# Kernel tuning notes

Hardware: AMD Instinct MI355X
Metric: run time of the kernel (lower is better)

Reference implementation:

```python
import jax, jax.numpy as jnp
import numpy as np

NUM_HEADS = 16
D_MODEL = 1024


def setup_inputs() -> dict:
    key = jax.random.key(0)
    k1, k2, k3 = jax.random.split(key, 3)
    x = jax.random.normal(k1, (4, 2048, D_MODEL), dtype=jnp.float32)
    # torch.nn.Linear weights are [out_features, in_features]
    w_qkv = jax.random.normal(k2, (3 * D_MODEL, D_MODEL), dtype=jnp.float32) * (1.0 / np.sqrt(D_MODEL))
    w_o = jax.random.normal(k3, (D_MODEL, D_MODEL), dtype=jnp.float32) * (1.0 / np.sqrt(D_MODEL))
    return {"x": x, "w_qkv": w_qkv, "w_o": w_o}


def reference(x, w_qkv, w_o):
    b, n, _ = x.shape
    h = NUM_HEADS
    dh = D_MODEL // h  # head dim
    qkv = jnp.einsum('bnd,ed->bne', x, w_qkv)            # (b, n, 3*d_model)
    # Faithful to: rearrange(qkv, 'b n (h d) -> b h n d', h=h) then chunk(3, dim=-1)
    qkv = qkv.reshape(b, n, h, 3 * dh).transpose(0, 2, 1, 3)  # (b, h, n, 3*dh)
    q, k, v = jnp.split(qkv, 3, axis=-1)                 # each (b, h, n, dh)
    scale = 1.0 / jnp.sqrt(jnp.asarray(dh, dtype=x.dtype))
    scores = jnp.einsum('bhqd,bhkd->bhqk', q, k) * scale  # (b, h, n, n)
    attn = jax.nn.softmax(scores, axis=-1)
    out = jnp.einsum('bhqk,bhkd->bhqd', attn, v)          # (b, h, n, dh)
    out = out.transpose(0, 2, 1, 3).reshape(b, n, h * dh)  # 'b h n d -> b n (h d)'
    return jnp.einsum('bnd,ed->bne', out, w_o)
```

## Files before the change

kernel.cpp:

```cpp
#include <hip/hip_runtime.h>

#define BATCH 4
#define SEQ 2048
#define DM 1024
#define NH 16
#define DH 64
#define M_TOT (BATCH * SEQ)
#define EQKV (3 * DM)
#define QSCALE 0.18033688011112042f

typedef __bf16 bf16x8 __attribute__((ext_vector_type(8)));
typedef unsigned short u16x8 __attribute__((ext_vector_type(8)));
typedef float f32x4 __attribute__((ext_vector_type(4)));
typedef float f32x16 __attribute__((ext_vector_type(16)));

static __device__ __forceinline__ unsigned short f2bf(float f) {
    unsigned int u = __builtin_bit_cast(unsigned int, f);
    u += 0x7fffu + ((u >> 16) & 1u);
    return (unsigned short)(u >> 16);
}

static __device__ __forceinline__ unsigned short f2bf_fast(float f) {
    return (unsigned short)((__builtin_bit_cast(unsigned int, f) + 0x8000u) >> 16);
}

static __device__ __forceinline__ unsigned int pkbf_fast(float a, float b) {
    unsigned int ua = __builtin_bit_cast(unsigned int, a) + 0x8000u;
    unsigned int ub = __builtin_bit_cast(unsigned int, b) + 0x8000u;
#if __has_builtin(__builtin_amdgcn_perm)
    return __builtin_amdgcn_perm(ub, ua, 0x07060302u);
#else
    return (ua >> 16) | (ub & 0xFFFF0000u);
#endif
}

static __device__ __forceinline__ float fast_exp2(float x) {
#if __has_builtin(__builtin_amdgcn_exp2f)
    return __builtin_amdgcn_exp2f(x);
#else
    return exp2f(x);
#endif
}

static __device__ __forceinline__ bf16x8 ld_frag(const ushort* p) {
    return *(const bf16x8*)p;
}

static __device__ __forceinline__ bf16x8 mk_frag(unsigned int a, unsigned int b,
                                                 unsigned int c, unsigned int d) {
    union { unsigned int u[4]; bf16x8 v; } t;
    t.u[0] = a; t.u[1] = b; t.u[2] = c; t.u[3] = d;
    return t.v;
}

__global__ __launch_bounds__(256) void detect_kernel(const ushort* __restrict__ x,
                                                     int* __restrict__ flag) {
    __shared__ int cnt[256];
    const int tid = threadIdx.x;
    int c = 0;
    for (int j = 0; j < 16; ++j) {
        unsigned short w = x[tid * 16 + j];
        int e = (w >> 7) & 0xFF;
        bool sane = (e == 0) || (e >= 0x60 && e <= 0x8F);
        c += sane ? 0 : 1;
    }
    cnt[tid] = c;
    __syncthreads();
    for (int s = 128; s > 0; s >>= 1) {
        if (tid < s) cnt[tid] += cnt[tid + s];
        __syncthreads();
    }
    if (tid == 0) flag[0] = (cnt[0] > 256) ? 1 : 0;
}

__global__ __launch_bounds__(256) void convert_frag_kernel(
    const void* __restrict__ src, ushort* __restrict__ dst, int R,
    const int* __restrict__ flag)
{
    const int t = blockIdx.x * 256 + threadIdx.x;
    if (t >= R * 128) return;
    const int m = t >> 7, kc = t & 127;

    u16x8 v;
    if (flag[0]) {
        const float* s = (const float*)src + (size_t)t * 8;
        #pragma unroll
        for (int j = 0; j < 8; ++j) v[j] = f2bf(s[j]);
    } else {
        v = *((const u16x8*)src + t);
    }
    const size_t o = (((size_t)(m >> 4) * 32 + (kc >> 2)) * 64 + (kc & 3) * 16 + (m & 15)) * 8;
    *(u16x8*)(dst + o) = v;
}

__global__ __launch_bounds__(256) void qkv_gemm_kernel(
    const ushort* __restrict__ XF, const ushort* __restrict__ WF,
    ushort* __restrict__ QF, ushort* __restrict__ KF, ushort* __restrict__ VF)
{
    const int lane = threadIdx.x & 63;
    const int wave = threadIdx.x >> 6;
    const int col  = lane & 15;
    const int quad = lane >> 4;
    const int m0 = blockIdx.y * 128 + (wave >> 1) * 64;
    const int e0 = blockIdx.x * 128 + (wave & 1) * 64;
    const int mt0 = m0 >> 4, et0 = e0 >> 4;

    f32x4 acc[4][4];
    #pragma unroll
    for (int i = 0; i < 4; ++i)
        #pragma unroll
        for (int j = 0; j < 4; ++j) acc[i][j] = f32x4{0.f, 0.f, 0.f, 0.f};

    for (int kt = 0; kt < 32; ++kt) {
        bf16x8 a[4], b[4];
        #pragma unroll
        for (int i = 0; i < 4; ++i) {
            a[i] = ld_frag(XF + ((size_t)((mt0 + i) * 32 + kt) * 64 + lane) * 8);
            b[i] = ld_frag(WF + ((size_t)((et0 + i) * 32 + kt) * 64 + lane) * 8);
        }
        #pragma unroll
        for (int i = 0; i < 4; ++i)
            #pragma unroll
            for (int j = 0; j < 4; ++j)
                acc[i][j] = __builtin_amdgcn_mfma_f32_16x16x32_bf16(a[i], b[j], acc[i][j], 0, 0, 0);
    }

    #pragma unroll
    for (int ej = 0; ej < 4; ++ej) {
        const int e = e0 + ej * 16 + col;
        const int h = e / 192;
        const int c = e - h * 192;
        #pragma unroll
        for (int mi = 0; mi < 4; ++mi) {
            #pragma unroll
            for (int r = 0; r < 4; ++r) {
                const int m = m0 + mi * 16 + quad * 4 + r;
                const int bh = (m >> 11) * NH + h;
                const int n = m & (SEQ - 1);
                const float val = acc[mi][ej][r];
                if (c < 64) {
                    const int d = c;
                    QF[(((size_t)(bh * 64 + (n >> 5)) * 4 + (d >> 4)) * 64
                        + ((d >> 3) & 1) * 32 + (n & 31)) * 8 + (d & 7)] = f2bf_fast(val * QSCALE);
                } else if (c < 128) {
                    const int d = c - 64;
                    KF[(((size_t)(bh * 64 + (n >> 5)) * 4 + (d >> 4)) * 64
                        + ((d >> 3) & 1) * 32 + (n & 31)) * 8 + (d & 7)] = f2bf_fast(val);
                } else {
                    const int d = c - 128;
                    const int r4 = n & 15;
                    const int s4 = (r4 & 3) | (((r4 >> 3) & 1) << 2) | (((r4 >> 2) & 1) << 3);
                    VF[((((size_t)(bh * 32 + (n >> 6)) * 2 + (d >> 5)) * 4 + ((n >> 4) & 3)) * 64
                        + (s4 >> 3) * 32 + (d & 31)) * 8 + (s4 & 7)] = f2bf_fast(val);
                }
            }
        }
    }
}

__global__ __launch_bounds__(256) void attn_kernel(
    const ushort* __restrict__ QF, const ushort* __restrict__ KF,
    const ushort* __restrict__ VF, ushort* __restrict__ AOF)
{
    __shared__ float lred[2][33][64];

    const int lane = threadIdx.x & 63;
    const int wave = threadIdx.x >> 6;
    const int half = lane >> 5;
    const int l31  = lane & 31;

    const int i = blockIdx.x;
    const int xcd = i & 7;
    const int s = i >> 3;
    const int qc = s & 31;
    const int bh = ((s >> 5) << 3) | xcd;
    const int qt  = wave & 1;
    const int kvh = wave >> 1;
    const int q0 = qc * 64 + qt * 32;

    const ushort* qfb = QF + ((size_t)(bh * 64 + (q0 >> 5)) * 4) * 512;
    bf16x8 bq[4];
    #pragma unroll
    for (int d4 = 0; d4 < 4; ++d4) bq[d4] = ld_frag(qfb + d4 * 512 + lane * 8);

    const ushort* kfb = KF + (size_t)bh * 131072 + (size_t)kvh * 65536;
    const ushort* vfb = VF + (size_t)bh * 131072 + (size_t)kvh * 65536;

    float l_i = 0.f;
    f32x16 acc0 = {}, acc1 = {};

    for (int it = 0; it < 16; ++it) {
        const ushort* vp = vfb + (size_t)it * 4096;
        bf16x8 va0[4], va1[4];
        #pragma unroll
        for (int f4 = 0; f4 < 4; ++f4) {
            va0[f4] = ld_frag(vp + f4 * 512 + lane * 8);
            va1[f4] = ld_frag(vp + (4 + f4) * 512 + lane * 8);
        }

        f32x16 st0 = {}, st1 = {};
        const ushort* kp = kfb + (size_t)it * 4096;
        #pragma unroll
        for (int d4 = 0; d4 < 4; ++d4) {
            bf16x8 ka0 = ld_frag(kp + d4 * 512 + lane * 8);
            bf16x8 ka1 = ld_frag(kp + (4 + d4) * 512 + lane * 8);
            st0 = __builtin_amdgcn_mfma_f32_32x32x16_bf16(ka0, bq[d4], st0, 0, 0, 0);
            st1 = __builtin_amdgcn_mfma_f32_32x32x16_bf16(ka1, bq[d4], st1, 0, 0, 0);
        }

        float rs = 0.f;
        #pragma unroll
        for (int t = 0; t < 16; ++t) { st0[t] = fast_exp2(st0[t]); rs += st0[t]; }
        #pragma unroll
        for (int t = 0; t < 16; ++t) { st1[t] = fast_exp2(st1[t]); rs += st1[t]; }
        l_i += rs;

        bf16x8 pf[4];
        pf[0] = mk_frag(pkbf_fast(st0[0],  st0[1]),  pkbf_fast(st0[2],  st0[3]),
                        pkbf_fast(st0[4],  st0[5]),  pkbf_fast(st0[6],  st0[7]));
        pf[1] = mk_frag(pkbf_fast(st0[8],  st0[9]),  pkbf_fast(st0[10], st0[11]),
                        pkbf_fast(st0[12], st0[13]), pkbf_fast(st0[14], st0[15]));
        pf[2] = mk_frag(pkbf_fast(st1[0],  st1[1]),  pkbf_fast(st1[2],  st1[3]),
                        pkbf_fast(st1[4],  st1[5]),  pkbf_fast(st1[6],  st1[7]));
        pf[3] = mk_frag(pkbf_fast(st1[8],  st1[9]),  pkbf_fast(st1[10], st1[11]),
                        pkbf_fast(st1[12], st1[13]), pkbf_fast(st1[14], st1[15]));

        #pragma unroll
        for (int f4 = 0; f4 < 4; ++f4) {
            acc0 = __builtin_amdgcn_mfma_f32_32x32x16_bf16(va0[f4], pf[f4], acc0, 0, 0, 0);
            acc1 = __builtin_amdgcn_mfma_f32_32x32x16_bf16(va1[f4], pf[f4], acc1, 0, 0, 0);
        }
    }

    l_i += __shfl_xor(l_i, 32, 64);

    if (kvh == 1) {
        #pragma unroll
        for (int r = 0; r < 16; ++r) {
            lred[qt][r][lane]      = acc0[r];
            lred[qt][16 + r][lane] = acc1[r];
        }
        lred[qt][32][lane] = l_i;
    }
    __syncthreads();
    if (kvh == 0) {
        #pragma unroll
        for (int r = 0; r < 16; ++r) {
            acc0[r] += lred[qt][r][lane];
            acc1[r] += lred[qt][16 + r][lane];
        }
        l_i += lred[qt][32][lane];

        const int b = bh >> 4, h = bh & (NH - 1);
        const float inv = 1.f / l_i;
        const int n_g = b * SEQ + q0 + l31;
        #pragma unroll
        for (int r = 0; r < 16; ++r) {
            const int d = (r & 3) + 8 * (r >> 2) + 4 * half;
            #pragma unroll
            for (int p = 0; p < 2; ++p) {
                const int e = h * 64 + p * 32 + d;
                const float val = (p == 0 ? acc0[r] : acc1[r]) * inv;
                AOF[(((size_t)(n_g >> 4) * 32 + (e >> 5)) * 64
                     + ((e >> 3) & 3) * 16 + (n_g & 15)) * 8 + (e & 7)] = f2bf_fast(val);
            }
        }
    }
}

__global__ __launch_bounds__(256) void out_gemm_kernel(
    const ushort* __restrict__ AOF, const ushort* __restrict__ WOF,
    void* __restrict__ out, const int* __restrict__ flag)
{
    const int lane = threadIdx.x & 63;
    const int wave = threadIdx.x >> 6;
    const int col  = lane & 15;
    const int quad = lane >> 4;
    const int m0 = blockIdx.y * 128 + (wave >> 1) * 64;
    const int e0 = blockIdx.x * 128 + (wave & 1) * 64;
    const int mt0 = m0 >> 4, et0 = e0 >> 4;
    const int f = flag[0];

    f32x4 acc[4][4];
    #pragma unroll
    for (int i = 0; i < 4; ++i)
        #pragma unroll
        for (int j = 0; j < 4; ++j) acc[i][j] = f32x4{0.f, 0.f, 0.f, 0.f};

    for (int kt = 0; kt < 32; ++kt) {
        bf16x8 a[4], b[4];
        #pragma unroll
        for (int i = 0; i < 4; ++i) {
            a[i] = ld_frag(AOF + ((size_t)((mt0 + i) * 32 + kt) * 64 + lane) * 8);
            b[i] = ld_frag(WOF + ((size_t)((et0 + i) * 32 + kt) * 64 + lane) * 8);
        }
        #pragma unroll
        for (int i = 0; i < 4; ++i)
            #pragma unroll
            for (int j = 0; j < 4; ++j)
                acc[i][j] = __builtin_amdgcn_mfma_f32_16x16x32_bf16(a[i], b[j], acc[i][j], 0, 0, 0);
    }

    if (f == 0) {
        ushort* o = (ushort*)out;
        #pragma unroll
        for (int mi = 0; mi < 4; ++mi)
            #pragma unroll
            for (int ej = 0; ej < 4; ++ej)
                #pragma unroll
                for (int r = 0; r < 4; ++r)
                    o[(size_t)(m0 + mi * 16 + quad * 4 + r) * DM + e0 + ej * 16 + col] = f2bf_fast(acc[mi][ej][r]);
    } else {
        float* o = (float*)out;
        #pragma unroll
        for (int mi = 0; mi < 4; ++mi)
            #pragma unroll
            for (int ej = 0; ej < 4; ++ej)
                #pragma unroll
                for (int r = 0; r < 4; ++r)
                    o[(size_t)(m0 + mi * 16 + quad * 4 + r) * DM + e0 + ej * 16 + col] = acc[mi][ej][r];
    }
}

extern "C" void kernel_launch(void* const* d_in, const int* in_sizes, int n_in,
                              void* d_out, int out_size, void* d_ws, size_t ws_size,
                              hipStream_t stream) {
    const void* x_raw     = d_in[0];
    const void* w_qkv_raw = d_in[1];
    const void* w_o_raw   = d_in[2];

    char* ws = (char*)d_ws;
    int*    flag  = (int*)ws;
    ushort* XF    = (ushort*)(ws + 256);
    ushort* WQKVF = (ushort*)(ws + 256 + (16u << 20));
    ushort* WOF   = (ushort*)(ws + 256 + (22u << 20));
    ushort* QF    = (ushort*)(ws + 256 + (24u << 20));
    ushort* KF    = (ushort*)(ws + 256 + (40u << 20));
    ushort* VF    = (ushort*)(ws + 256 + (56u << 20));
    ushort* AOF   = XF;

    detect_kernel<<<1, 256, 0, stream>>>((const ushort*)x_raw, flag);
    convert_frag_kernel<<<M_TOT / 2, 256, 0, stream>>>(x_raw, XF, M_TOT, flag);
    convert_frag_kernel<<<EQKV / 2, 256, 0, stream>>>(w_qkv_raw, WQKVF, EQKV, flag);
    convert_frag_kernel<<<DM / 2, 256, 0, stream>>>(w_o_raw, WOF, DM, flag);

    qkv_gemm_kernel<<<dim3(EQKV / 128, M_TOT / 128), 256, 0, stream>>>(XF, WQKVF, QF, KF, VF);
    attn_kernel<<<dim3(BATCH * NH * (SEQ / 64)), 256, 0, stream>>>(QF, KF, VF, AOF);
    out_gemm_kernel<<<dim3(DM / 128, M_TOT / 128), 256, 0, stream>>>(AOF, WOF, d_out, flag);
}
```

Measured before the change: 302.8 us.

## Swizzle GEMM block order per XCD and use packed bf16 convert and adds

Both projection GEMMs remap block indices so that blocks landing on the same XCD work on a contiguous tile region, which aims to improve L2 reuse of the operand tiles. In the attention kernel, the bf16 packing of the exp2 probabilities now uses the hardware v_cvt_pk_bf16_f32 instruction instead of manual bit arithmetic. The row-sum accumulation uses packed v_pk_add_f32 across four partial accumulators, which cuts VALU instruction count and shortens the dependency chain. Rounding changes from round-half-up to the hardware's rounding mode, and the ordering of the sum changes slightly.

```diff
diff --git a/kernel.cpp b/kernel.cpp
--- a/kernel.cpp
+++ b/kernel.cpp
@@ -11,6 +11,7 @@
 
 typedef __bf16 bf16x8 __attribute__((ext_vector_type(8)));
 typedef unsigned short u16x8 __attribute__((ext_vector_type(8)));
+typedef float f32x2 __attribute__((ext_vector_type(2)));
 typedef float f32x4 __attribute__((ext_vector_type(4)));
 typedef float f32x16 __attribute__((ext_vector_type(16)));
 
@@ -24,14 +25,16 @@
     return (unsigned short)((__builtin_bit_cast(unsigned int, f) + 0x8000u) >> 16);
 }
 
-static __device__ __forceinline__ unsigned int pkbf_fast(float a, float b) {
-    unsigned int ua = __builtin_bit_cast(unsigned int, a) + 0x8000u;
-    unsigned int ub = __builtin_bit_cast(unsigned int, b) + 0x8000u;
-#if __has_builtin(__builtin_amdgcn_perm)
-    return __builtin_amdgcn_perm(ub, ua, 0x07060302u);
-#else
-    return (ua >> 16) | (ub & 0xFFFF0000u);
-#endif
+static __device__ __forceinline__ unsigned int cvt_pk_bf16(float lo, float hi) {
+    unsigned int r;
+    asm("v_cvt_pk_bf16_f32 %0, %1, %2" : "=v"(r) : "v"(lo), "v"(hi));
+    return r;
+}
+
+static __device__ __forceinline__ f32x2 pk_add(f32x2 a, f32x2 b) {
+    f32x2 d;
+    asm("v_pk_add_f32 %0, %1, %2" : "=v"(d) : "v"(a), "v"(b));
+    return d;
 }
 
 static __device__ __forceinline__ float fast_exp2(float x) {
@@ -101,8 +104,12 @@
     const int wave = threadIdx.x >> 6;
     const int col  = lane & 15;
     const int quad = lane >> 4;
-    const int m0 = blockIdx.y * 128 + (wave >> 1) * 64;
-    const int e0 = blockIdx.x * 128 + (wave & 1) * 64;
+    const int orig = blockIdx.y * 24 + blockIdx.x;
+    const int sid  = (orig & 7) * 192 + (orig >> 3);
+    const int bx = sid % 24;
+    const int by = sid / 24;
+    const int m0 = by * 128 + (wave >> 1) * 64;
+    const int e0 = bx * 128 + (wave & 1) * 64;
     const int mt0 = m0 >> 4, et0 = e0 >> 4;
 
     f32x4 acc[4][4];
@@ -186,8 +193,19 @@
     const ushort* kfb = KF + (size_t)bh * 131072 + (size_t)kvh * 65536;
     const ushort* vfb = VF + (size_t)bh * 131072 + (size_t)kvh * 65536;
 
-    float l_i = 0.f;
+    f32x2 lp0 = {0.f, 0.f}, lp1 = {0.f, 0.f}, lp2 = {0.f, 0.f}, lp3 = {0.f, 0.f};
     f32x16 acc0 = {}, acc1 = {};
+
+#define LACC(v) do { \
+        lp0 = pk_add(lp0, __builtin_shufflevector(v, v, 0, 1));   \
+        lp1 = pk_add(lp1, __builtin_shufflevector(v, v, 2, 3));   \
+        lp2 = pk_add(lp2, __builtin_shufflevector(v, v, 4, 5));   \
+        lp3 = pk_add(lp3, __builtin_shufflevector(v, v, 6, 7));   \
+        lp0 = pk_add(lp0, __builtin_shufflevector(v, v, 8, 9));   \
+        lp1 = pk_add(lp1, __builtin_shufflevector(v, v, 10, 11)); \
+        lp2 = pk_add(lp2, __builtin_shufflevector(v, v, 12, 13)); \
+        lp3 = pk_add(lp3, __builtin_shufflevector(v, v, 14, 15)); \
+    } while (0)
 
     for (int it = 0; it < 16; ++it) {
         const ushort* vp = vfb + (size_t)it * 4096;
@@ -208,22 +226,22 @@
             st1 = __builtin_amdgcn_mfma_f32_32x32x16_bf16(ka1, bq[d4], st1, 0, 0, 0);
         }
 
-        float rs = 0.f;
-        #pragma unroll
-        for (int t = 0; t < 16; ++t) { st0[t] = fast_exp2(st0[t]); rs += st0[t]; }
-        #pragma unroll
-        for (int t = 0; t < 16; ++t) { st1[t] = fast_exp2(st1[t]); rs += st1[t]; }
-        l_i += rs;
+        #pragma unroll
+        for (int t = 0; t < 16; ++t) st0[t] = fast_exp2(st0[t]);
+        #pragma unroll
+        for (int t = 0; t < 16; ++t) st1[t] = fast_exp2(st1[t]);
+        LACC(st0);
+        LACC(st1);
 
         bf16x8 pf[4];
-        pf[0] = mk_frag(pkbf_fast(st0[0],  st0[1]),  pkbf_fast(st0[2],  st0[3]),
-                        pkbf_fast(st0[4],  st0[5]),  pkbf_fast(st0[6],  st0[7]));
-        pf[1] = mk_frag(pkbf_fast(st0[8],  st0[9]),  pkbf_fast(st0[10], st0[11]),
-                        pkbf_fast(st0[12], st0[13]), pkbf_fast(st0[14], st0[15]));
-        pf[2] = mk_frag(pkbf_fast(st1[0],  st1[1]),  pkbf_fast(st1[2],  st1[3]),
-                        pkbf_fast(st1[4],  st1[5]),  pkbf_fast(st1[6],  st1[7]));
-        pf[3] = mk_frag(pkbf_fast(st1[8],  st1[9]),  pkbf_fast(st1[10], st1[11]),
-                        pkbf_fast(st1[12], st1[13]), pkbf_fast(st1[14], st1[15]));
+        pf[0] = mk_frag(cvt_pk_bf16(st0[0],  st0[1]),  cvt_pk_bf16(st0[2],  st0[3]),
+                        cvt_pk_bf16(st0[4],  st0[5]),  cvt_pk_bf16(st0[6],  st0[7]));
+        pf[1] = mk_frag(cvt_pk_bf16(st0[8],  st0[9]),  cvt_pk_bf16(st0[10], st0[11]),
+                        cvt_pk_bf16(st0[12], st0[13]), cvt_pk_bf16(st0[14], st0[15]));
+        pf[2] = mk_frag(cvt_pk_bf16(st1[0],  st1[1]),  cvt_pk_bf16(st1[2],  st1[3]),
+                        cvt_pk_bf16(st1[4],  st1[5]),  cvt_pk_bf16(st1[6],  st1[7]));
+        pf[3] = mk_frag(cvt_pk_bf16(st1[8],  st1[9]),  cvt_pk_bf16(st1[10], st1[11]),
+                        cvt_pk_bf16(st1[12], st1[13]), cvt_pk_bf16(st1[14], st1[15]));
 
         #pragma unroll
         for (int f4 = 0; f4 < 4; ++f4) {
@@ -231,6 +249,10 @@
             acc1 = __builtin_amdgcn_mfma_f32_32x32x16_bf16(va1[f4], pf[f4], acc1, 0, 0, 0);
         }
     }
+#undef LACC
+
+    f32x2 lt = pk_add(pk_add(lp0, lp1), pk_add(lp2, lp3));
+    float l_i = lt[0] + lt[1];
 
     l_i += __shfl_xor(l_i, 32, 64);
 
@@ -276,8 +298,12 @@
     const int wave = threadIdx.x >> 6;
     const int col  = lane & 15;
     const int quad = lane >> 4;
-    const int m0 = blockIdx.y * 128 + (wave >> 1) * 64;
-    const int e0 = blockIdx.x * 128 + (wave & 1) * 64;
+    const int orig = blockIdx.y * 8 + blockIdx.x;
+    const int sid  = (orig & 7) * 64 + (orig >> 3);
+    const int bx = sid & 7;
+    const int by = sid >> 3;
+    const int m0 = by * 128 + (wave >> 1) * 64;
+    const int e0 = bx * 128 + (wave & 1) * 64;
     const int mt0 = m0 >> 4, et0 = e0 >> 4;
     const int f = flag[0];
 
```

New measurement: 309.1 us. 1.02x slower.
